# Kernel optimization log

Measured on AMD Instinct MI355X. Metric: run time of the kernel, lower is better.

Reference implementation:

```python
import jax, jax.numpy as jnp
import numpy as np

B, T, H, W = 2, 20, 56, 56
WIN = 8
NUM_THROWS = 64
UNITS = 64


def setup_inputs() -> dict:
    key = jax.random.key(0)
    cnt = [0]
    def nk():
        cnt[0] += 1
        return jax.random.fold_in(key, cnt[0])
    def rn(shape, fan):
        return jax.random.normal(nk(), shape, jnp.float32) / np.sqrt(float(fan))
    d = {}
    d["inputs"] = jax.random.uniform(nk(), (B, T, H, W, 3), dtype=jnp.float32)
    for name, cin, cout in [("c11", 3, 32), ("c12", 32, 32), ("c21", 32, 64), ("c22", 64, 64), ("c31", 64, 128), ("c32", 128, 128)]:
        d[name + "_k"] = rn((3, 3, 3, cin, cout), 27 * cin)
        d[name + "_b"] = 0.1 * rn((cout,), 1)
    for name, fin in [("g1", 128), ("g2", UNITS), ("g3", UNITS)]:
        d[name + "_wx"] = rn((fin, 3 * UNITS), fin)
        d[name + "_wh"] = rn((UNITS, 3 * UNITS), UNITS)
        d[name + "_b"] = 0.1 * rn((2, 3 * UNITS), 1)
    for name, fin, fout in [("d1", 64, 64), ("d2", 64, 32), ("thr", 32, NUM_THROWS), ("tori", 32, 2)]:
        d[name + "_w"] = rn((fin, fout), fin)
        d[name + "_b"] = 0.1 * rn((fout,), 1)
    return d


def _conv(x, k, b):
    # Conv3D, padding='same', relu. x: (N, D, H, W, Cin), k: (3,3,3,Cin,Cout)
    y = jax.lax.conv_general_dilated(x, k, (1, 1, 1), "SAME", dimension_numbers=("NDHWC", "DHWIO", "NDHWC"))
    return jax.nn.relu(y + b)


def _pool(x):
    # MaxPooling3D((1,2,2)), valid padding
    return jax.lax.reduce_window(x, -jnp.inf, jax.lax.max, (1, 1, 2, 2, 1), (1, 1, 2, 2, 1), "VALID")


def _gru(x, wx, wh, b, return_seq):
    # Keras GRU (reset_after=True). Gate order [z, r, h]; b: (2, 3U) = (input bias, recurrent bias)
    U = wh.shape[0]
    xp = jnp.einsum("bti,ij->btj", x, wx) + b[0]  # precompute input projection
    def step(h, xt):
        rec = h @ wh + b[1]
        z = jax.nn.sigmoid(xt[:, :U] + rec[:, :U])
        r = jax.nn.sigmoid(xt[:, U:2 * U] + rec[:, U:2 * U])
        hh = jnp.tanh(xt[:, 2 * U:] + r * rec[:, 2 * U:])
        hn = z * h + (1.0 - z) * hh
        return hn, hn
    h0 = jnp.zeros((x.shape[0], U), x.dtype)
    hT, seq = jax.lax.scan(step, h0, jnp.swapaxes(xp, 0, 1))
    return jnp.swapaxes(seq, 0, 1) if return_seq else hT


def _forward(inputs, c11_k, c11_b, c12_k, c12_b, c21_k, c21_b, c22_k, c22_b, c31_k, c31_b, c32_k, c32_b, g1_wx, g1_wh, g1_b, g2_wx, g2_wh, g2_b, g3_wx, g3_wh, g3_b, d1_w, d1_b, d2_w, d2_b, thr_w, thr_b, tori_w, tori_b):
    def cnn(block):
        x = _conv(block, c11_k, c11_b)
        x = _conv(x, c12_k, c12_b)
        x = _pool(x)
        x = _conv(x, c21_k, c21_b)
        x = _conv(x, c22_k, c22_b)
        x = _pool(x)
        x = _conv(x, c31_k, c31_b)
        x = _conv(x, c32_k, c32_b)
        return jnp.mean(x, axis=(1, 2, 3))  # GlobalAveragePooling3D
    newT = inputs.shape[1] - WIN + 1
    # stride-1 overlapping windows (tf.image.extract_patches equivalent)
    idx = jnp.arange(newT)[:, None] + jnp.arange(WIN)[None, :]
    wins = jnp.swapaxes(inputs[:, idx], 0, 1)
    feats = jnp.swapaxes(jax.lax.map(cnn, wins), 0, 1)  # (B, newT, 128)
    x = _gru(feats, g1_wx, g1_wh, g1_b, True)
    x = _gru(x, g2_wx, g2_wh, g2_b, True)
    h = _gru(x, g3_wx, g3_wh, g3_b, False)  # (B, 64)
    h = jax.nn.relu(h @ d1_w + d1_b)
    h = jax.nn.relu(h @ d2_w + d2_b)
    throw = jax.nn.softmax(h @ thr_w + thr_b, axis=-1)
    tori = jax.nn.softmax(h @ tori_w + tori_b, axis=-1)
    return throw, tori


def reference(inputs, c11_k, c11_b, c12_k, c12_b, c21_k, c21_b, c22_k, c22_b, c31_k, c31_b, c32_k, c32_b, g1_wx, g1_wh, g1_b, g2_wx, g2_wh, g2_b, g3_wx, g3_wh, g3_b, d1_w, d1_b, d2_w, d2_b, thr_w, thr_b, tori_w, tori_b):
    return _forward(inputs, c11_k, c11_b, c12_k, c12_b, c21_k, c21_b, c22_k, c22_b, c31_k, c31_b, c32_k, c32_b, g1_wx, g1_wh, g1_b, g2_wx, g2_wh, g2_b, g3_wx, g3_wh, g3_b, d1_w, d1_b, d2_w, d2_b, thr_w, thr_b, tori_w, tori_b)
```

## Files before the change

kernel.cpp:

```cpp
#include <hip/hip_runtime.h>
#include <math.h>

#define DD 8

typedef __attribute__((ext_vector_type(8))) short short8v;
typedef __attribute__((ext_vector_type(4))) float f32x4;

__device__ __forceinline__ float4 ld4(const float* p) {
    return *reinterpret_cast<const float4*>(p);
}
__device__ __forceinline__ void st4(float* p, float4 v) {
    *reinterpret_cast<float4*>(p) = v;
}
__device__ __forceinline__ void fma4(float4& a, float s, float4 w) {
    a.x = fmaf(s, w.x, a.x);
    a.y = fmaf(s, w.y, a.y);
    a.z = fmaf(s, w.z, a.z);
    a.w = fmaf(s, w.w, a.w);
}
__device__ __forceinline__ float sigmoidf(float x) { return 1.f / (1.f + expf(-x)); }

__device__ __forceinline__ float bf2f(unsigned short u) {
    union { unsigned int i; float f; } v; v.i = ((unsigned int)u) << 16; return v.f;
}
__device__ __forceinline__ unsigned short f2bf(float f) {
    union { float f; unsigned int i; } v; v.f = f;
    unsigned int r = v.i + 0x7FFFu + ((v.i >> 16) & 1u);
    return (unsigned short)(r >> 16);
}

__global__ __launch_bounds__(256)
void pack_w_k(const float* __restrict__ wgt, unsigned short* __restrict__ pk,
              int chunks, int cout_n, int total)
{
    for (int id = blockIdx.x * 256 + threadIdx.x; id < total; id += gridDim.x * 256) {
        int j = id & 7;
        int l = (id >> 3) & 63;
        int rest = id >> 9;
        int chunk = rest % chunks;
        int nt = rest / chunks;
        int k = chunk * 32 + ((l >> 4) << 3) + j;
        int cout = nt * 16 + (l & 15);
        pk[id] = f2bf(wgt[(size_t)k * cout_n + cout]);
    }
}

__global__ __launch_bounds__(256)
void conv_c11_k(const float* __restrict__ in, const float* __restrict__ wgt,
                const float* __restrict__ bias, unsigned short* __restrict__ out, int b)
{
    constexpr int HH = 56, WW = 56, WP = 58, COUT = 32, HR = 4, SR = HR + 2;
    __shared__ float wlds[27 * 3 * 32];
    __shared__ float slab[3 * SR * WP * 3];
    const int blk = blockIdx.x;
    const int hg = blk % 14;
    const int d = (blk / 14) % DD;
    const int n = blk / (14 * DD);
    const int h0 = hg * HR;
    const int tx = threadIdx.x, ty = threadIdx.y;
    const int tid = ty * 64 + tx;

    for (int i = tid; i < 27 * 3 * 32; i += 256) wlds[i] = wgt[i];
    for (int i = tid; i < 3 * SR * WP * 3; i += 256) {
        int ci = i % 3;
        int rest = i / 3;
        int wp = rest % WP; rest /= WP;
        int r = rest % SR;
        int f = rest / SR;
        int d2 = d + f - 1;
        int h2 = h0 + r - 1;
        int w = wp - 1;
        float v = 0.f;
        if (d2 >= 0 && d2 < DD && h2 >= 0 && h2 < HH && w >= 0 && w < WW) {
            int frame = b * 20 + n + d2;
            v = in[(((size_t)frame * HH + h2) * WW + w) * 3 + ci];
        }
        slab[i] = v;
    }
    __syncthreads();

    const int c0 = ty * 8;
    if (tx < WW) {
        float4 a0[HR], a1[HR];
        #pragma unroll
        for (int hh = 0; hh < HR; ++hh) {
            a0[hh] = float4{0, 0, 0, 0};
            a1[hh] = float4{0, 0, 0, 0};
        }
        #pragma unroll
        for (int f = 0; f < 3; ++f) {
            #pragma unroll
            for (int kh = 0; kh < 3; ++kh) {
                #pragma unroll
                for (int kw = 0; kw < 3; ++kw) {
                    const float* wr = &wlds[((f * 9 + kh * 3 + kw) * 3) * 32 + c0];
                    float4 w0a = ld4(wr);            float4 w0b = ld4(wr + 4);
                    float4 w1a = ld4(wr + 32);       float4 w1b = ld4(wr + 36);
                    float4 w2a = ld4(wr + 64);       float4 w2b = ld4(wr + 68);
                    #pragma unroll
                    for (int hh = 0; hh < HR; ++hh) {
                        const float* lr = &slab[((f * SR + hh + kh) * WP + tx + kw) * 3];
                        float s0 = lr[0], s1 = lr[1], s2 = lr[2];
                        fma4(a0[hh], s0, w0a); fma4(a1[hh], s0, w0b);
                        fma4(a0[hh], s1, w1a); fma4(a1[hh], s1, w1b);
                        fma4(a0[hh], s2, w2a); fma4(a1[hh], s2, w2b);
                    }
                }
            }
        }
        float4 ba = ld4(bias + c0), bb = ld4(bias + c0 + 4);
        #pragma unroll
        for (int hh = 0; hh < HR; ++hh) {
            unsigned short o[8];
            o[0] = f2bf(fmaxf(0.f, a0[hh].x + ba.x));
            o[1] = f2bf(fmaxf(0.f, a0[hh].y + ba.y));
            o[2] = f2bf(fmaxf(0.f, a0[hh].z + ba.z));
            o[3] = f2bf(fmaxf(0.f, a0[hh].w + ba.w));
            o[4] = f2bf(fmaxf(0.f, a1[hh].x + bb.x));
            o[5] = f2bf(fmaxf(0.f, a1[hh].y + bb.y));
            o[6] = f2bf(fmaxf(0.f, a1[hh].z + bb.z));
            o[7] = f2bf(fmaxf(0.f, a1[hh].w + bb.w));
            size_t ob = ((((size_t)n * DD + d) * HH + (h0 + hh)) * WW + tx) * COUT + c0;
            *(short8v*)&out[ob] = *(short8v*)o;
        }
    }
}

template<int CIN, int COUT, int H, int W, int HROWS, int MW, int NW>
__global__ __launch_bounds__(256)
void convmf_k(const unsigned short* __restrict__ act,
              const unsigned short* __restrict__ pk,
              const float* __restrict__ bias,
              unsigned short* __restrict__ out)
{
    constexpr int CPT = CIN / 32;
    constexpr int CHUNKS = 27 * CPT;
    constexpr int KH = HROWS + 2;
    constexpr int ROWS = 3 * KH;
    constexpr int WP = W + 2;
    constexpr int CINP = CIN + 8;
    constexpr int TPH = (W + 15) / 16;
    constexpr int MTILES = HROWS * TPH;
    constexpr int NTILES = COUT / 16;
    constexpr int MGROUPS = MTILES / MW;
    constexpr int LDSE = ROWS * WP * CINP;
    static_assert(MTILES % MW == 0 && NTILES % NW == 0, "tile divisibility");
    static_assert(MGROUPS * (NTILES / NW) == 4, "4-wave coverage");
    __shared__ __align__(16) short sh[LDSE + 512];

    const int HB = H / HROWS;
    const int blk = blockIdx.x;
    const int hblk = blk % HB;
    const int d = (blk / HB) % DD;
    const int bn = blk / (HB * DD);
    const int h0 = hblk * HROWS;
    const int tid = threadIdx.x;
    const int lane = tid & 63;
    const int wave = tid >> 6;
    const int l15 = lane & 15;
    const int l4 = lane >> 4;

    constexpr int C8 = CIN / 8;
    constexpr int V8R = WP * C8;
    for (int i = tid; i < ROWS * V8R; i += 256) {
        int r = i / V8R;
        int q = i - r * V8R;
        int wp_ = q / C8;
        int co = (q - wp_ * C8) * 8;
        int kd = r / KH, khh = r - kd * KH;
        int dp = d + kd - 1, hp = h0 + khh - 1;
        int w = wp_ - 1;
        short8v v = short8v{0, 0, 0, 0, 0, 0, 0, 0};
        if (dp >= 0 && dp < DD && hp >= 0 && hp < H && w >= 0 && w < W)
            v = *(const short8v*)&act[((((size_t)bn * DD + dp) * H + hp) * W + w) * CIN + co];
        *(short8v*)&sh[(r * WP + wp_) * CINP + co] = v;
    }
    __syncthreads();

    const int mg = wave % MGROUPS;
    const int ng = wave / MGROUPS;

    f32x4 acc[MW][NW];
    #pragma unroll
    for (int mi = 0; mi < MW; ++mi)
        #pragma unroll
        for (int ni = 0; ni < NW; ++ni)
            acc[mi][ni] = f32x4{0.f, 0.f, 0.f, 0.f};

    const short8v* bp = (const short8v*)pk;
    #pragma unroll 1
    for (int tap = 0; tap < 27; ++tap) {
        const int kd = tap / 9;
        const int rm = tap - kd * 9;
        const int kh = rm / 3;
        const int kw = rm - kh * 3;
        int abase[MW];
        #pragma unroll
        for (int mi = 0; mi < MW; ++mi) {
            const int mt = mg * MW + mi;
            const int row = kd * KH + kh + mt / TPH;
            const int wp = (mt % TPH) * 16 + l15 + kw;
            abase[mi] = (row * WP + wp) * CINP + l4 * 8;
        }
        #pragma unroll
        for (int cp = 0; cp < CPT; ++cp) {
            const int chunk = tap * CPT + cp;
            short8v a[MW], b[NW];
            #pragma unroll
            for (int mi = 0; mi < MW; ++mi)
                a[mi] = *(const short8v*)&sh[abase[mi] + cp * 32];
            #pragma unroll
            for (int ni = 0; ni < NW; ++ni)
                b[ni] = bp[((size_t)(ng * NW + ni) * CHUNKS + chunk) * 64 + lane];
            #pragma unroll
            for (int mi = 0; mi < MW; ++mi)
                #pragma unroll
                for (int ni = 0; ni < NW; ++ni)
                    acc[mi][ni] = __builtin_amdgcn_mfma_f32_16x16x32_bf16(a[mi], b[ni], acc[mi][ni], 0, 0, 0);
        }
    }

    #pragma unroll
    for (int mi = 0; mi < MW; ++mi) {
        const int mt = mg * MW + mi;
        const int hout = h0 + mt / TPH;
        const int wbase = (mt % TPH) * 16 + l4 * 4;
        #pragma unroll
        for (int ni = 0; ni < NW; ++ni) {
            const int cout = (ng * NW + ni) * 16 + l15;
            const float bi = bias[cout];
            #pragma unroll
            for (int r = 0; r < 4; ++r) {
                const int w = wbase + r;
                if (w < W) {
                    float v = fmaxf(0.f, acc[mi][ni][r] + bi);
                    out[((((size_t)bn * DD + d) * H + hout) * W + w) * COUT + cout] = f2bf(v);
                }
            }
        }
    }
}

template<int C, int HO, int WO>
__global__ __launch_bounds__(256)
void poolb_k(const unsigned short* __restrict__ in, unsigned short* __restrict__ out,
             int total8, size_t obase)
{
    constexpr int C8 = C / 8;
    for (int idx = blockIdx.x * 256 + threadIdx.x; idx < total8; idx += gridDim.x * 256) {
        int c8 = idx % C8;
        int t = idx / C8;
        int wo = t % WO; t /= WO;
        int ho = t % HO; t /= HO;
        size_t base = (((size_t)t * (2 * HO) + 2 * ho) * (2 * WO) + 2 * wo) * C + c8 * 8;
        short8v a = *(const short8v*)&in[base];
        short8v b = *(const short8v*)&in[base + C];
        short8v c = *(const short8v*)&in[base + (size_t)(2 * WO) * C];
        short8v e = *(const short8v*)&in[base + (size_t)(2 * WO) * C + C];
        unsigned short o[8];
        #pragma unroll
        for (int j = 0; j < 8; ++j) {
            unsigned short av = (unsigned short)a[j], bv = (unsigned short)b[j];
            unsigned short cv = (unsigned short)c[j], ev = (unsigned short)e[j];
            unsigned short m1 = av > bv ? av : bv;
            unsigned short m2 = cv > ev ? cv : ev;
            o[j] = m1 > m2 ? m1 : m2;
        }
        *(short8v*)&out[obase + (size_t)idx * 8] = *(short8v*)o;
    }
}

__global__ __launch_bounds__(1024)
void gapb_k(const unsigned short* __restrict__ in, float* __restrict__ outf)
{
    __shared__ float part[8][128];
    const int n = blockIdx.x;
    const int c = threadIdx.x;
    const int dy = threadIdx.y;
    float s = 0.f;
    const unsigned short* p = &in[((size_t)n * 1568 + dy * 196) * 128 + c];
    #pragma unroll 4
    for (int i = 0; i < 196; ++i) s += bf2f(p[(size_t)i * 128]);
    part[dy][c] = s;
    __syncthreads();
    if (dy == 0) {
        float t = 0.f;
        #pragma unroll
        for (int k = 0; k < 8; ++k) t += part[k][c];
        outf[n * 128 + c] = t * (1.f / 1568.f);
    }
}

__global__ __launch_bounds__(192)
void xp1_k(const float* __restrict__ feats, const float* __restrict__ wx,
           const float* __restrict__ gb, float* __restrict__ xp1)
{
    __shared__ float xrow[128];
    const int tb = blockIdx.x;
    const int b = tb & 1, t = tb >> 1;
    const int j = threadIdx.x;
    if (j < 128) xrow[j] = feats[(b * 13 + t) * 128 + j];
    __syncthreads();
    float s = gb[j];
    #pragma unroll 16
    for (int k = 0; k < 128; ++k) s = fmaf(xrow[k], wx[k * 192 + j], s);
    xp1[tb * 192 + j] = s;
}

__global__ __launch_bounds__(384)
void gru2_k(const float* __restrict__ xp1,
            const float* __restrict__ g1_wh, const float* __restrict__ g1_b,
            const float* __restrict__ g2_wx, const float* __restrict__ g2_wh, const float* __restrict__ g2_b,
            const float* __restrict__ g3_wx, const float* __restrict__ g3_wh, const float* __restrict__ g3_b,
            const float* __restrict__ d1_w, const float* __restrict__ d1_b,
            const float* __restrict__ d2_w, const float* __restrict__ d2_b,
            const float* __restrict__ thr_w, const float* __restrict__ thr_b,
            const float* __restrict__ tori_w, const float* __restrict__ tori_b,
            float* __restrict__ out)
{
    __shared__ float xp[13 * 2 * 192];
    __shared__ float seq[26 * 64];
    __shared__ unsigned short wbuf[64 * 192];
    __shared__ float hbuf[2 * 64];
    __shared__ float rec[2 * 192];
    __shared__ float gbr[192];
    __shared__ float tmp[2 * 64];
    __shared__ float hd2[2 * 32];
    __shared__ float red[4];
    __shared__ float tl[4];
    const int tid = threadIdx.x;
    const int jj = tid % 192;
    const int bb = tid / 192;

    for (int i = tid; i < 13 * 2 * 192; i += 384) xp[i] = xp1[i];

    const float* WHs[3] = {g1_wh, g2_wh, g3_wh};
    const float* WXs[3] = {nullptr, g2_wx, g3_wx};
    const float* GBs[3] = {g1_b, g2_b, g3_b};

    for (int layer = 0; layer < 3; ++layer) {
        const float* gb = GBs[layer];
        if (layer > 0) {
            const float* wx = WXs[layer];
            for (int i = tid; i < 64 * 192; i += 384) wbuf[i] = f2bf(wx[i]);
            __syncthreads();
            const float bi = gb[jj];
            for (int t = 0; t < 13; ++t) {
                const float* xr = &seq[(bb * 13 + t) * 64];
                float s = bi;
                #pragma unroll 8
                for (int k = 0; k < 64; ++k) s = fmaf(xr[k], bf2f(wbuf[k * 192 + jj]), s);
                xp[(t * 2 + bb) * 192 + jj] = s;
            }
            __syncthreads();
        }
        const float* wh = WHs[layer];
        for (int i = tid; i < 64 * 192; i += 384) wbuf[i] = f2bf(wh[i]);
        if (tid < 192) gbr[tid] = gb[192 + tid];
        if (tid < 128) hbuf[tid] = 0.f;
        __syncthreads();
        for (int t = 0; t < 13; ++t) {
            {
                const float* hr = &hbuf[bb * 64];
                float s = gbr[jj];
                #pragma unroll 8
                for (int k = 0; k < 64; ++k) s = fmaf(hr[k], bf2f(wbuf[k * 192 + jj]), s);
                rec[tid] = s;
            }
            __syncthreads();
            if (tid < 128) {
                int b = tid / 64, u = tid % 64;
                const float* xpt = &xp[(t * 2 + b) * 192];
                const float* rc = &rec[b * 192];
                float z = sigmoidf(xpt[u] + rc[u]);
                float r = sigmoidf(xpt[64 + u] + rc[64 + u]);
                float hh = tanhf(xpt[128 + u] + r * rc[128 + u]);
                float hn = z * hbuf[b * 64 + u] + (1.f - z) * hh;
                hbuf[b * 64 + u] = hn;
                seq[(b * 13 + t) * 64 + u] = hn;
            }
            __syncthreads();
        }
    }

    if (tid < 128) {
        int b = tid / 64, u = tid % 64;
        float s = d1_b[u];
        for (int k = 0; k < 64; ++k) s = fmaf(hbuf[b * 64 + k], d1_w[k * 64 + u], s);
        tmp[b * 64 + u] = fmaxf(s, 0.f);
    }
    __syncthreads();
    if (tid < 64) {
        int b = tid / 32, u = tid % 32;
        float s = d2_b[u];
        for (int k = 0; k < 64; ++k) s = fmaf(tmp[b * 64 + k], d2_w[k * 32 + u], s);
        hd2[b * 32 + u] = fmaxf(s, 0.f);
    }
    __syncthreads();
    if (tid < 128) {
        int b = tid / 64, u = tid % 64;
        float s = thr_b[u];
        for (int k = 0; k < 32; ++k) s = fmaf(hd2[b * 32 + k], thr_w[k * 64 + u], s);
        tmp[b * 64 + u] = s;
    }
    if (tid >= 128 && tid < 132) {
        int i = tid - 128;
        int b = i >> 1, u = i & 1;
        float s = tori_b[u];
        for (int k = 0; k < 32; ++k) s = fmaf(hd2[b * 32 + k], tori_w[k * 2 + u], s);
        tl[i] = s;
    }
    __syncthreads();
    if (tid < 2) {
        float m = -1e30f;
        for (int u = 0; u < 64; ++u) m = fmaxf(m, tmp[tid * 64 + u]);
        float s = 0.f;
        for (int u = 0; u < 64; ++u) s += expf(tmp[tid * 64 + u] - m);
        red[tid * 2] = m;
        red[tid * 2 + 1] = s;
    }
    __syncthreads();
    if (tid < 128) {
        int b = tid >> 6;
        out[tid] = expf(tmp[tid] - red[b * 2]) / red[b * 2 + 1];
    }
    if (tid >= 128 && tid < 130) {
        int b = tid - 128;
        float a = tl[b * 2], c = tl[b * 2 + 1];
        float m = fmaxf(a, c);
        float e0 = expf(a - m), e1 = expf(c - m);
        float inv = 1.f / (e0 + e1);
        out[128 + b * 2 + 0] = e0 * inv;
        out[128 + b * 2 + 1] = e1 * inv;
    }
}

extern "C" void kernel_launch(void* const* d_in, const int* in_sizes, int n_in,
                              void* d_out, int out_size, void* d_ws, size_t ws_size,
                              hipStream_t stream) {
    const float* inputs = (const float*)d_in[0];
    const float* c11_k = (const float*)d_in[1];  const float* c11_b = (const float*)d_in[2];
    const float* c12_k = (const float*)d_in[3];  const float* c12_b = (const float*)d_in[4];
    const float* c21_k = (const float*)d_in[5];  const float* c21_b = (const float*)d_in[6];
    const float* c22_k = (const float*)d_in[7];  const float* c22_b = (const float*)d_in[8];
    const float* c31_k = (const float*)d_in[9];  const float* c31_b = (const float*)d_in[10];
    const float* c32_k = (const float*)d_in[11]; const float* c32_b = (const float*)d_in[12];
    const float* g1_wx = (const float*)d_in[13]; const float* g1_wh = (const float*)d_in[14]; const float* g1_b = (const float*)d_in[15];
    const float* g2_wx = (const float*)d_in[16]; const float* g2_wh = (const float*)d_in[17]; const float* g2_b = (const float*)d_in[18];
    const float* g3_wx = (const float*)d_in[19]; const float* g3_wh = (const float*)d_in[20]; const float* g3_b = (const float*)d_in[21];
    const float* d1_w = (const float*)d_in[22];  const float* d1_b = (const float*)d_in[23];
    const float* d2_w = (const float*)d_in[24];  const float* d2_b = (const float*)d_in[25];
    const float* thr_w = (const float*)d_in[26]; const float* thr_b = (const float*)d_in[27];
    const float* tori_w = (const float*)d_in[28]; const float* tori_b = (const float*)d_in[29];

    typedef unsigned short u16;
    char* base = (char*)d_ws;
    u16* pk12 = (u16*)base;
    u16* pk21 = pk12 + 27648;
    u16* pk22 = pk21 + 55296;
    u16* pk31 = pk22 + 110592;
    u16* pk32 = pk31 + 221184;
    float* feats = (float*)(base + 1714176);
    float* xp1   = (float*)(base + 1727488);
    u16* p1 = (u16*)(base + 1747456);
    u16* hA = (u16*)(base + 12184064);
    u16* hB = (u16*)(base + 33057280);
    float* out = (float*)d_out;

    pack_w_k<<<108, 256, 0, stream>>>(c12_k, pk12, 27, 32, 27648);
    pack_w_k<<<216, 256, 0, stream>>>(c21_k, pk21, 27, 64, 55296);
    pack_w_k<<<432, 256, 0, stream>>>(c22_k, pk22, 54, 64, 110592);
    pack_w_k<<<864, 256, 0, stream>>>(c31_k, pk31, 54, 128, 221184);
    pack_w_k<<<1728, 256, 0, stream>>>(c32_k, pk32, 108, 128, 442368);

    for (int b = 0; b < 2; ++b) {
        conv_c11_k<<<13 * 8 * 14, dim3(64, 4), 0, stream>>>(inputs, c11_k, c11_b, hA, b);
        convmf_k<32, 32, 56, 56, 1, 2, 1><<<13 * 8 * 56, 256, 0, stream>>>(hA, pk12, c12_b, hB);
        poolb_k<32, 28, 28><<<1274, 256, 0, stream>>>(hB, p1, 13 * 8 * 28 * 28 * 4, (size_t)b * 2609152);
    }
    convmf_k<32, 64, 28, 28, 2, 2, 2><<<26 * 8 * 14, 256, 0, stream>>>(p1, pk21, c21_b, hA);
    convmf_k<64, 64, 28, 28, 1, 2, 1><<<26 * 8 * 28, 256, 0, stream>>>(hA, pk22, c22_b, hB);
    poolb_k<64, 14, 14><<<1274, 256, 0, stream>>>(hB, p1, 26 * 8 * 14 * 14 * 8, 0);
    convmf_k<64, 128, 14, 14, 2, 2, 2><<<26 * 8 * 7, 256, 0, stream>>>(p1, pk31, c31_b, hA);
    convmf_k<128, 128, 14, 14, 2, 2, 2><<<26 * 8 * 7, 256, 0, stream>>>(hA, pk32, c32_b, hB);
    gapb_k<<<26, dim3(128, 8), 0, stream>>>(hB, feats);

    xp1_k<<<26, 192, 0, stream>>>(feats, g1_wx, g1_b, xp1);
    gru2_k<<<1, 384, 0, stream>>>(xp1,
        g1_wh, g1_b, g2_wx, g2_wh, g2_b, g3_wx, g3_wh, g3_b,
        d1_w, d1_b, d2_w, d2_b, thr_w, thr_b, tori_w, tori_b, out);
}
```

Before: 642.6 us.

## Merge weight-pack launches, unroll conv tap loop, split GRU dot-product accumulators

Five weight-packing kernel launches become one kernel that works out which tensor each index belongs to. The conv MFMA tap loop goes from unroll 1 to unroll 3 so the compiler can schedule loads across taps. The GRU matvec loops use four independent accumulators to shorten the serial FMA dependency chain on the latency-bound recurrent path. The extra unrolling may raise register pressure in the conv kernel and lower occupancy, and the reordered sums change float rounding slightly.

```diff
diff --git a/kernel.cpp b/kernel.cpp
--- a/kernel.cpp
+++ b/kernel.cpp
@@ -30,18 +30,25 @@
 }
 
 __global__ __launch_bounds__(256)
-void pack_w_k(const float* __restrict__ wgt, unsigned short* __restrict__ pk,
-              int chunks, int cout_n, int total)
-{
-    for (int id = blockIdx.x * 256 + threadIdx.x; id < total; id += gridDim.x * 256) {
-        int j = id & 7;
-        int l = (id >> 3) & 63;
-        int rest = id >> 9;
+void pack_all_k(const float* __restrict__ w12, const float* __restrict__ w21,
+                const float* __restrict__ w22, const float* __restrict__ w31,
+                const float* __restrict__ w32, unsigned short* __restrict__ pk)
+{
+    for (int id = blockIdx.x * 256 + threadIdx.x; id < 857088; id += gridDim.x * 256) {
+        const float* wgt; int chunks, coutn, local;
+        if (id < 27648)       { wgt = w12; chunks = 27;  coutn = 32;  local = id; }
+        else if (id < 82944)  { wgt = w21; chunks = 27;  coutn = 64;  local = id - 27648; }
+        else if (id < 193536) { wgt = w22; chunks = 54;  coutn = 64;  local = id - 82944; }
+        else if (id < 414720) { wgt = w31; chunks = 54;  coutn = 128; local = id - 193536; }
+        else                  { wgt = w32; chunks = 108; coutn = 128; local = id - 414720; }
+        int j = local & 7;
+        int l = (local >> 3) & 63;
+        int rest = local >> 9;
         int chunk = rest % chunks;
         int nt = rest / chunks;
         int k = chunk * 32 + ((l >> 4) << 3) + j;
         int cout = nt * 16 + (l & 15);
-        pk[id] = f2bf(wgt[(size_t)k * cout_n + cout]);
+        pk[id] = f2bf(wgt[(size_t)k * coutn + cout]);
     }
 }
 
@@ -188,7 +195,7 @@
             acc[mi][ni] = f32x4{0.f, 0.f, 0.f, 0.f};
 
     const short8v* bp = (const short8v*)pk;
-    #pragma unroll 1
+    #pragma unroll 3
     for (int tap = 0; tap < 27; ++tap) {
         const int kd = tap / 9;
         const int rm = tap - kd * 9;
@@ -347,10 +354,15 @@
             const float bi = gb[jj];
             for (int t = 0; t < 13; ++t) {
                 const float* xr = &seq[(bb * 13 + t) * 64];
-                float s = bi;
+                float s0 = 0.f, s1 = 0.f, s2 = 0.f, s3 = 0.f;
                 #pragma unroll 8
-                for (int k = 0; k < 64; ++k) s = fmaf(xr[k], bf2f(wbuf[k * 192 + jj]), s);
-                xp[(t * 2 + bb) * 192 + jj] = s;
+                for (int k = 0; k < 64; k += 4) {
+                    s0 = fmaf(xr[k + 0], bf2f(wbuf[(k + 0) * 192 + jj]), s0);
+                    s1 = fmaf(xr[k + 1], bf2f(wbuf[(k + 1) * 192 + jj]), s1);
+                    s2 = fmaf(xr[k + 2], bf2f(wbuf[(k + 2) * 192 + jj]), s2);
+                    s3 = fmaf(xr[k + 3], bf2f(wbuf[(k + 3) * 192 + jj]), s3);
+                }
+                xp[(t * 2 + bb) * 192 + jj] = bi + ((s0 + s1) + (s2 + s3));
             }
             __syncthreads();
         }
@@ -362,10 +374,15 @@
         for (int t = 0; t < 13; ++t) {
             {
                 const float* hr = &hbuf[bb * 64];
-                float s = gbr[jj];
+                float s0 = 0.f, s1 = 0.f, s2 = 0.f, s3 = 0.f;
                 #pragma unroll 8
-                for (int k = 0; k < 64; ++k) s = fmaf(hr[k], bf2f(wbuf[k * 192 + jj]), s);
-                rec[tid] = s;
+                for (int k = 0; k < 64; k += 4) {
+                    s0 = fmaf(hr[k + 0], bf2f(wbuf[(k + 0) * 192 + jj]), s0);
+                    s1 = fmaf(hr[k + 1], bf2f(wbuf[(k + 1) * 192 + jj]), s1);
+                    s2 = fmaf(hr[k + 2], bf2f(wbuf[(k + 2) * 192 + jj]), s2);
+                    s3 = fmaf(hr[k + 3], bf2f(wbuf[(k + 3) * 192 + jj]), s3);
+                }
+                rec[tid] = gbr[jj] + ((s0 + s1) + (s2 + s3));
             }
             __syncthreads();
             if (tid < 128) {
@@ -455,11 +472,12 @@
 
     typedef unsigned short u16;
     char* base = (char*)d_ws;
-    u16* pk12 = (u16*)base;
-    u16* pk21 = pk12 + 27648;
-    u16* pk22 = pk21 + 55296;
-    u16* pk31 = pk22 + 110592;
-    u16* pk32 = pk31 + 221184;
+    u16* pkall = (u16*)base;
+    u16* pk12 = pkall;
+    u16* pk21 = pkall + 27648;
+    u16* pk22 = pkall + 82944;
+    u16* pk31 = pkall + 193536;
+    u16* pk32 = pkall + 414720;
     float* feats = (float*)(base + 1714176);
     float* xp1   = (float*)(base + 1727488);
     u16* p1 = (u16*)(base + 1747456);
@@ -467,11 +485,7 @@
     u16* hB = (u16*)(base + 33057280);
     float* out = (float*)d_out;
 
-    pack_w_k<<<108, 256, 0, stream>>>(c12_k, pk12, 27, 32, 27648);
-    pack_w_k<<<216, 256, 0, stream>>>(c21_k, pk21, 27, 64, 55296);
-    pack_w_k<<<432, 256, 0, stream>>>(c22_k, pk22, 54, 64, 110592);
-    pack_w_k<<<864, 256, 0, stream>>>(c31_k, pk31, 54, 128, 221184);
-    pack_w_k<<<1728, 256, 0, stream>>>(c32_k, pk32, 108, 128, 442368);
+    pack_all_k<<<1674, 256, 0, stream>>>(c12_k, c21_k, c22_k, c31_k, c32_k, pkall);
 
     for (int b = 0; b < 2; ++b) {
         conv_c11_k<<<13 * 8 * 14, dim3(64, 4), 0, stream>>>(inputs, c11_k, c11_b, hA, b);
```

After: 594.1 us. -7.6%, faster.
